# Optimization experiments

Hardware: AMD Instinct MI355X
Metric: run time of the kernel (lower is better)

Reference implementation:

```python
import jax, jax.numpy as jnp
import numpy as np

# ---- static geometry (matches init_kwargs / input_specs) ----
WH, WW = 7, 7            # window_size
H, W = 112, 112          # feature-map size (reshape[1], reshape[2])
NH = 8                   # num_heads
EPS = 1e-5


def _relative_position_index():
    ch, cw = np.arange(WH), np.arange(WW)
    coords = np.stack(np.meshgrid(ch, cw, indexing='ij')).reshape(2, -1)   # (2, S)
    rel = coords[:, :, None] - coords[:, None, :]                          # (2, S, S)
    rel = rel.transpose(1, 2, 0).astype(np.int64)
    rel[..., 0] += WH - 1
    rel[..., 1] += WW - 1
    rel[..., 0] *= 2 * WW - 1
    return rel.sum(-1)                                                     # (S, S)


def _shift_mask():
    h, w = H // WH, W // WW
    s1, s2 = WH - WH // 2, WW - WW // 2
    m = np.zeros((h, w, WH, WW, WH, WW), dtype=bool)
    m[-1, :, :s1, :, s1:, :] = True
    m[-1, :, s1:, :, :s1, :] = True
    m[:, -1, :, :s2, :, s2:] = True
    m[:, -1, :, s2:, :, :s2] = True
    return m.reshape(1, 1, h * w, WH * WW, WH * WW)                        # (1,1,N,S,S)


REL_IDX = jnp.asarray(_relative_position_index())
ATTN_MASK = jnp.asarray(_shift_mask())


def layernorm(x, g, b):
    mu = x.mean(-1, keepdims=True)
    var = jnp.mean(jnp.square(x - mu), -1, keepdims=True)
    return (x - mu) * jax.lax.rsqrt(var + EPS) * g + b


def setup_inputs() -> dict:
    key = jax.random.key(0)
    ks = jax.random.split(key, 8)
    B, N, S, C = 8, 256, 49, 256
    d = {
        'x': jax.random.normal(ks[0], (B, N, S, C), jnp.float32),
        'reshape': jnp.array([B, H, W, C], jnp.int64),
        'norm1_g': jnp.ones((C,), jnp.float32),
        'norm1_b': jnp.zeros((C,), jnp.float32),
        'qkv_w': jax.random.normal(ks[1], (3 * C, C), jnp.float32) * 0.02,
        'qkv_b': jnp.zeros((3 * C,), jnp.float32),
        'proj_w': jax.random.normal(ks[2], (C, C), jnp.float32) * 0.02,
        'proj_b': jnp.zeros((C,), jnp.float32),
        'norm2_g': jnp.ones((C,), jnp.float32),
        'norm2_b': jnp.zeros((C,), jnp.float32),
        'mlp_w1': jax.random.normal(ks[3], (4 * C, C), jnp.float32) * 0.02,
        'mlp_b1': jnp.zeros((4 * C,), jnp.float32),
        'mlp_w2': jax.random.normal(ks[4], (C, 4 * C), jnp.float32) * 0.02,
        'mlp_b2': jnp.zeros((C,), jnp.float32),
        'bias_table': jax.random.normal(ks[5], ((2 * WH - 1) * (2 * WW - 1), NH), jnp.float32) * 0.02,
    }
    return d


def reference(x, reshape, norm1_g, norm1_b, qkv_w, qkv_b, proj_w, proj_b,
              norm2_g, norm2_b, mlp_w1, mlp_b1, mlp_w2, mlp_b2, bias_table):
    B, N, S, C = x.shape
    hd = C // NH
    scale = hd ** -0.5

    shortcut = x
    h = layernorm(x, norm1_g, norm1_b)
    qkv = h @ qkv_w.T + qkv_b                                   # (B,N,S,3C)
    qkv = qkv.reshape(B, N, S, 3, NH, hd).transpose(3, 0, 4, 1, 2, 5)
    q, k, v = qkv[0], qkv[1], qkv[2]                            # (B,NH,N,S,hd)

    attn = jnp.einsum('bhnsd,bhntd->bhnst', q * scale, k)       # (B,NH,N,S,S)
    bias = bias_table[REL_IDX]                                  # (S,S,NH) gather
    attn = attn + bias.transpose(2, 0, 1)[None, :, None]        # +(1,NH,1,S,S)
    attn = jnp.where(ATTN_MASK, -jnp.inf, attn)                 # type=='S' mask
    attn = jax.nn.softmax(attn, axis=-1)

    out = jnp.einsum('bhnst,bhntd->bhnsd', attn, v)             # (B,NH,N,S,hd)
    out = out.transpose(0, 2, 3, 1, 4).reshape(B, N, S, C)
    out = out @ proj_w.T + proj_b

    x = shortcut + out
    h2 = layernorm(x, norm2_g, norm2_b)
    mlp = jax.nn.gelu(h2 @ mlp_w1.T + mlp_b1, approximate=False) @ mlp_w2.T + mlp_b2
    return x + mlp
```

## Files before the change

### kernel.cpp

```cpp
#include <hip/hip_runtime.h>
#include <hip/hip_bf16.h>
#include <math.h>

#define R_TOTAL 100352
#define CDIM    256
#define NWIN    2048
#define NHEAD   8
#define HD      32
#define SW      49

typedef short s8v  __attribute__((ext_vector_type(8)));
typedef float f32x4 __attribute__((ext_vector_type(4)));

__device__ __forceinline__ unsigned short f2bf(float f) {
    __hip_bfloat16 h = __float2bfloat16(f);
    return *reinterpret_cast<unsigned short*>(&h);
}

__device__ __forceinline__ void gload_lds16(const void* g, void* lds) {
    __builtin_amdgcn_global_load_lds(
        (const __attribute__((address_space(1))) void*)g,
        (__attribute__((address_space(3))) void*)lds, 16, 0, 0);
}

__global__ void cvt_f32_bf16(const float* __restrict__ in,
                             unsigned short* __restrict__ out, int n4) {
    int i = blockIdx.x * blockDim.x + threadIdx.x;
    if (i < n4) {
        float4 v = ((const float4*)in)[i];
        unsigned short o[4] = {f2bf(v.x), f2bf(v.y), f2bf(v.z), f2bf(v.w)};
        ((uint2*)out)[i] = *(uint2*)o;
    }
}

__global__ __launch_bounds__(256)
void ln_rows(const float* __restrict__ in, const float* __restrict__ g,
             const float* __restrict__ b, unsigned short* __restrict__ out,
             int rows) {
    int wid = threadIdx.x >> 6, lane = threadIdx.x & 63;
    int row = blockIdx.x * 4 + wid;
    if (row >= rows) return;
    const float4 v = *(const float4*)(in + (size_t)row * CDIM + lane * 4);
    float s = v.x + v.y + v.z + v.w;
#pragma unroll
    for (int t = 1; t < 64; t <<= 1) s += __shfl_xor(s, t);
    float mean = s * (1.0f / 256.0f);
    float dx = v.x - mean, dy = v.y - mean, dz = v.z - mean, dw = v.w - mean;
    float q = dx * dx + dy * dy + dz * dz + dw * dw;
#pragma unroll
    for (int t = 1; t < 64; t <<= 1) q += __shfl_xor(q, t);
    float r = rsqrtf(q * (1.0f / 256.0f) + 1e-5f);
    const float4 gg = *(const float4*)(g + lane * 4);
    const float4 bb = *(const float4*)(b + lane * 4);
    unsigned short o[4] = {f2bf(dx * r * gg.x + bb.x), f2bf(dy * r * gg.y + bb.y),
                           f2bf(dz * r * gg.z + bb.z), f2bf(dw * r * gg.w + bb.w)};
    *(uint2*)(out + (size_t)row * CDIM + lane * 4) = *(uint2*)o;
}

template <int EPI>
__global__ __launch_bounds__(256)
void gemm_nt(const unsigned short* __restrict__ A, const unsigned short* __restrict__ B,
             const float* __restrict__ bias, const float* __restrict__ resid,
             void* __restrict__ outp, int M, int N, int K) {
    constexpr int BM = 128, BN = 128, BK = 32;
    __shared__ unsigned short As[BM][BK];
    __shared__ unsigned short Bs[BN][BK];

    const int tiles_n = N / BN;
    const int bm = blockIdx.x / tiles_n;
    const int bn = blockIdx.x % tiles_n;
    const int tid = threadIdx.x;
    const int wid = tid >> 6;
    const int lane = tid & 63;
    const int wr = wid >> 1, wc = wid & 1;
    const int fr = lane & 15;
    const int kc = lane >> 4;

    f32x4 acc[4][4] = {};

    const int srow = wid * 16 + (lane >> 2);
    const int scol = (lane & 3) * 8;
    const unsigned short* Abase = A + (size_t)(bm * BM) * K + scol;
    const unsigned short* Bbase = B + (size_t)(bn * BN) * K + scol;
    char* AsB = (char*)&As[0][0];
    char* BsB = (char*)&Bs[0][0];
    const int lbase = wid * 1024;

    for (int kt = 0; kt < K; kt += BK) {
        gload_lds16(Abase + (size_t)srow * K + kt,        AsB + lbase);
        gload_lds16(Abase + (size_t)(srow + 64) * K + kt, AsB + 4096 + lbase);
        gload_lds16(Bbase + (size_t)srow * K + kt,        BsB + lbase);
        gload_lds16(Bbase + (size_t)(srow + 64) * K + kt, BsB + 4096 + lbase);
        __syncthreads();
        s8v af[4], bfr[4];
#pragma unroll
        for (int i = 0; i < 4; ++i) af[i]  = *(const s8v*)&As[wr * 64 + i * 16 + fr][kc * 8];
#pragma unroll
        for (int j = 0; j < 4; ++j) bfr[j] = *(const s8v*)&Bs[wc * 64 + j * 16 + fr][kc * 8];
#pragma unroll
        for (int i = 0; i < 4; ++i)
#pragma unroll
            for (int j = 0; j < 4; ++j)
                acc[i][j] = __builtin_amdgcn_mfma_f32_16x16x32_bf16(af[i], bfr[j], acc[i][j], 0, 0, 0);
        __syncthreads();
    }

    const int m0 = bm * BM + wr * 64;
    const int n0 = bn * BN + wc * 64;
#pragma unroll
    for (int i = 0; i < 4; ++i) {
#pragma unroll
        for (int j = 0; j < 4; ++j) {
#pragma unroll
            for (int v = 0; v < 4; ++v) {
                const int m = m0 + i * 16 + kc * 4 + v;
                const int n = n0 + j * 16 + fr;
                float val = acc[i][j][v] + bias[n];
                if constexpr (EPI == 0) {
                    const int part = n >> 8;
                    const int c = n & 255;
                    const int head = c >> 5;
                    const int dd = c & 31;
                    const int win = m / SW;
                    const int s = m - win * SW;
                    ((unsigned short*)outp)[(size_t)part * ((size_t)NWIN * NHEAD * SW * HD)
                        + (((size_t)(win * NHEAD + head) * SW + s) * HD) + dd] = f2bf(val);
                } else if constexpr (EPI == 1) {
                    ((float*)outp)[(size_t)m * CDIM + n] = val + resid[(size_t)m * CDIM + n];
                } else if constexpr (EPI == 2) {
                    float gv = 0.5f * val * (1.0f + erff(val * 0.70710678118654752f));
                    ((unsigned short*)outp)[(size_t)m * 1024 + n] = f2bf(gv);
                } else {
                    ((float*)outp)[(size_t)m * CDIM + n] = val + resid[(size_t)m * CDIM + n];
                }
            }
        }
    }
}

__global__ __launch_bounds__(64)
void attn_win(const unsigned short* __restrict__ qkv,
              const float* __restrict__ btab,
              unsigned short* __restrict__ outp)
{
    __shared__ unsigned short Vt[32][72];
    __shared__ unsigned short Ps[64][72];
    __shared__ float bcol[169];

    const int wh = blockIdx.x;
    const int win = wh >> 3;
    const int head = wh & 7;
    const int lane = threadIdx.x;
    const size_t s3 = (size_t)NWIN * NHEAD * SW * HD;
    const size_t base = (size_t)wh * (SW * HD);

    for (int t = lane; t < 169; t += 64) bcol[t] = btab[t * NHEAD + head];

    {
        const int r = lane;
        if (r < SW) {
            const int4* v4 = (const int4*)(qkv + 2 * s3 + base + (size_t)r * HD);
            int4 vt[4];
#pragma unroll
            for (int c = 0; c < 4; ++c) vt[c] = v4[c];
            const unsigned short* vr = (const unsigned short*)vt;
#pragma unroll
            for (int d = 0; d < 32; ++d) Vt[d][r] = vr[d];
        } else {
#pragma unroll
            for (int d = 0; d < 32; ++d) Vt[d][r] = 0;
        }
    }

    const int fr = lane & 15, kc = lane >> 4;

    s8v qa[4], kb[4];
    {
        const unsigned short* Qg = qkv + base;
        const unsigned short* Kg = qkv + s3 + base;
#pragma unroll
        for (int i = 0; i < 4; ++i)
            qa[i] = *(const s8v*)(Qg + (size_t)(i * 16 + fr) * HD + kc * 8);
#pragma unroll
        for (int j = 0; j < 4; ++j)
            kb[j] = *(const s8v*)(Kg + (size_t)(j * 16 + fr) * HD + kc * 8);
    }

    f32x4 sc[4][4] = {};
#pragma unroll
    for (int i = 0; i < 4; ++i)
#pragma unroll
        for (int j = 0; j < 4; ++j)
            sc[i][j] = __builtin_amdgcn_mfma_f32_16x16x32_bf16(qa[i], kb[j], sc[i][j], 0, 0, 0);

    __syncthreads();

    const float scale = 0.17677669529663687f;
    const int nwin = win & 255;
    const bool lastrow = ((nwin >> 4) == 15);
    const bool lastcol = ((nwin & 15) == 15);

    int cj[4];
    bool jh4[4], jw4[4], jvalid[4];
#pragma unroll
    for (int tj = 0; tj < 4; ++tj) {
        const int j = tj * 16 + fr;
        const int jh = j / 7, jw = j - jh * 7;
        jvalid[tj] = (j < SW);
        cj[tj] = jh * 13 + jw;
        jh4[tj] = (jh < 4);
        jw4[tj] = (jw < 4);
    }

#pragma unroll
    for (int ti = 0; ti < 4; ++ti) {
#pragma unroll
        for (int v = 0; v < 4; ++v) {
            const int i = ti * 16 + kc * 4 + v;
            const int ih = i / 7, iw = i - ih * 7;
            const bool ivalid = (i < SW);
            const int ci = ih * 13 + iw;
            const bool ih4 = (ih < 4), iw4 = (iw < 4);
            float vals[4];
#pragma unroll
            for (int tj = 0; tj < 4; ++tj) {
                const bool ok = ivalid && jvalid[tj];
                const int bidx = ok ? (ci - cj[tj] + 84) : 0;
                const float bv = bcol[bidx];
                const bool msk = (lastrow && (ih4 != jh4[tj])) ||
                                 (lastcol && (iw4 != jw4[tj]));
                const float s = sc[ti][tj][v] * scale + bv;
                vals[tj] = (ok && !msk) ? s : -1e30f;
            }
            float mx = fmaxf(fmaxf(vals[0], vals[1]), fmaxf(vals[2], vals[3]));
#pragma unroll
            for (int t = 1; t < 16; t <<= 1) mx = fmaxf(mx, __shfl_xor(mx, t));
            float e[4], sum = 0.0f;
#pragma unroll
            for (int tj = 0; tj < 4; ++tj) { e[tj] = __expf(vals[tj] - mx); sum += e[tj]; }
#pragma unroll
            for (int t = 1; t < 16; t <<= 1) sum += __shfl_xor(sum, t);
            const float inv = 1.0f / sum;
#pragma unroll
            for (int tj = 0; tj < 4; ++tj)
                Ps[i][tj * 16 + fr] = f2bf(e[tj] * inv);
        }
    }
    __syncthreads();

    f32x4 oa[4][2] = {};
#pragma unroll
    for (int ks = 0; ks < 2; ++ks) {
        s8v pa[4], vb[2];
#pragma unroll
        for (int ti = 0; ti < 4; ++ti) pa[ti] = *(const s8v*)&Ps[ti * 16 + fr][ks * 32 + kc * 8];
#pragma unroll
        for (int tj = 0; tj < 2; ++tj) vb[tj] = *(const s8v*)&Vt[tj * 16 + fr][ks * 32 + kc * 8];
#pragma unroll
        for (int ti = 0; ti < 4; ++ti)
#pragma unroll
            for (int tj = 0; tj < 2; ++tj)
                oa[ti][tj] = __builtin_amdgcn_mfma_f32_16x16x32_bf16(pa[ti], vb[tj], oa[ti][tj], 0, 0, 0);
    }

#pragma unroll
    for (int ti = 0; ti < 4; ++ti)
#pragma unroll
        for (int tj = 0; tj < 2; ++tj)
#pragma unroll
            for (int v = 0; v < 4; ++v) {
                const int i = ti * 16 + kc * 4 + v;
                if (i < SW) {
                    const int d = tj * 16 + fr;
                    outp[((size_t)win * SW + i) * CDIM + head * HD + d] = f2bf(oa[ti][tj][v]);
                }
            }
}

extern "C" void kernel_launch(void* const* d_in, const int* in_sizes, int n_in,
                              void* d_out, int out_size, void* d_ws, size_t ws_size,
                              hipStream_t stream) {
    const float* x       = (const float*)d_in[0];
    const float* n1g     = (const float*)d_in[2];
    const float* n1b     = (const float*)d_in[3];
    const float* qkv_w   = (const float*)d_in[4];
    const float* qkv_b   = (const float*)d_in[5];
    const float* proj_w  = (const float*)d_in[6];
    const float* proj_b  = (const float*)d_in[7];
    const float* n2g     = (const float*)d_in[8];
    const float* n2b     = (const float*)d_in[9];
    const float* mlp_w1  = (const float*)d_in[10];
    const float* mlp_b1  = (const float*)d_in[11];
    const float* mlp_w2  = (const float*)d_in[12];
    const float* mlp_b2  = (const float*)d_in[13];
    const float* btab    = (const float*)d_in[14];

    const int R = R_TOTAL;

    char* w = (char*)d_ws;
    unsigned short* wqkv  = (unsigned short*)w; w += (size_t)768 * 256 * 2;
    unsigned short* wproj = (unsigned short*)w; w += (size_t)256 * 256 * 2;
    unsigned short* wm1   = (unsigned short*)w; w += (size_t)1024 * 256 * 2;
    unsigned short* wm2   = (unsigned short*)w; w += (size_t)256 * 1024 * 2;
    unsigned short* hbuf  = (unsigned short*)w; w += (size_t)R * CDIM * 2;
    unsigned short* qkvb  = (unsigned short*)w;
    unsigned short* hid   = qkvb;               w += (size_t)3 * R * CDIM * 2;
    unsigned short* attno = (unsigned short*)w; w += (size_t)R * CDIM * 2;
    float*          x2    = (float*)w;          w += (size_t)R * CDIM * 4;
    unsigned short* h2    = hbuf;

    cvt_f32_bf16<<<192, 256, 0, stream>>>(qkv_w,  wqkv, 49152);
    cvt_f32_bf16<<<64,  256, 0, stream>>>(proj_w, wproj, 16384);
    cvt_f32_bf16<<<256, 256, 0, stream>>>(mlp_w1, wm1, 65536);
    cvt_f32_bf16<<<256, 256, 0, stream>>>(mlp_w2, wm2, 65536);

    ln_rows<<<R / 4, 256, 0, stream>>>(x, n1g, n1b, hbuf, R);

    gemm_nt<0><<<784 * 6, 256, 0, stream>>>(hbuf, wqkv, qkv_b, nullptr, qkvb, R, 768, 256);

    attn_win<<<NWIN * NHEAD, 64, 0, stream>>>(qkvb, btab, attno);

    gemm_nt<1><<<784 * 2, 256, 0, stream>>>(attno, wproj, proj_b, x, x2, R, 256, 256);

    ln_rows<<<R / 4, 256, 0, stream>>>(x2, n2g, n2b, h2, R);

    gemm_nt<2><<<784 * 8, 256, 0, stream>>>(h2, wm1, mlp_b1, nullptr, hid, R, 1024, 256);

    gemm_nt<3><<<784 * 2, 256, 0, stream>>>(hid, wm2, mlp_b2, x2, (float*)d_out, R, 256, 1024);
}
```

Baseline: 751.5 us.

## Double-buffer GEMM LDS tiles and swizzle block order across XCDs

```diff
diff --git a/kernel.cpp b/kernel.cpp
--- a/kernel.cpp
+++ b/kernel.cpp
@@ -58,17 +58,22 @@
 }
 
 template <int EPI>
-__global__ __launch_bounds__(256)
+__global__ __launch_bounds__(256, 4)
 void gemm_nt(const unsigned short* __restrict__ A, const unsigned short* __restrict__ B,
              const float* __restrict__ bias, const float* __restrict__ resid,
              void* __restrict__ outp, int M, int N, int K) {
     constexpr int BM = 128, BN = 128, BK = 32;
-    __shared__ unsigned short As[BM][BK];
-    __shared__ unsigned short Bs[BN][BK];
+    __shared__ unsigned short As[2][BM][BK];
+    __shared__ unsigned short Bs[2][BN][BK];
+
+    const int nwg = gridDim.x;
+    const int cpx = nwg >> 3;
+    const int bid = blockIdx.x;
+    const int swz = (bid & 7) * cpx + (bid >> 3);
 
     const int tiles_n = N / BN;
-    const int bm = blockIdx.x / tiles_n;
-    const int bn = blockIdx.x % tiles_n;
+    const int bm = swz / tiles_n;
+    const int bn = swz % tiles_n;
     const int tid = threadIdx.x;
     const int wid = tid >> 6;
     const int lane = tid & 63;
@@ -82,28 +87,41 @@
     const int scol = (lane & 3) * 8;
     const unsigned short* Abase = A + (size_t)(bm * BM) * K + scol;
     const unsigned short* Bbase = B + (size_t)(bn * BN) * K + scol;
-    char* AsB = (char*)&As[0][0];
-    char* BsB = (char*)&Bs[0][0];
+    char* AsB = (char*)&As[0][0][0];
+    char* BsB = (char*)&Bs[0][0][0];
     const int lbase = wid * 1024;
 
-    for (int kt = 0; kt < K; kt += BK) {
-        gload_lds16(Abase + (size_t)srow * K + kt,        AsB + lbase);
-        gload_lds16(Abase + (size_t)(srow + 64) * K + kt, AsB + 4096 + lbase);
-        gload_lds16(Bbase + (size_t)srow * K + kt,        BsB + lbase);
-        gload_lds16(Bbase + (size_t)(srow + 64) * K + kt, BsB + 4096 + lbase);
-        __syncthreads();
+    auto stage = [&](int buf, int kt) {
+        char* Ad = AsB + buf * 8192 + lbase;
+        char* Bd = BsB + buf * 8192 + lbase;
+        gload_lds16(Abase + (size_t)srow * K + kt,        Ad);
+        gload_lds16(Abase + (size_t)(srow + 64) * K + kt, Ad + 4096);
+        gload_lds16(Bbase + (size_t)srow * K + kt,        Bd);
+        gload_lds16(Bbase + (size_t)(srow + 64) * K + kt, Bd + 4096);
+    };
+    auto compute = [&](int buf) {
         s8v af[4], bfr[4];
 #pragma unroll
-        for (int i = 0; i < 4; ++i) af[i]  = *(const s8v*)&As[wr * 64 + i * 16 + fr][kc * 8];
-#pragma unroll
-        for (int j = 0; j < 4; ++j) bfr[j] = *(const s8v*)&Bs[wc * 64 + j * 16 + fr][kc * 8];
+        for (int i = 0; i < 4; ++i) af[i]  = *(const s8v*)&As[buf][wr * 64 + i * 16 + fr][kc * 8];
+#pragma unroll
+        for (int j = 0; j < 4; ++j) bfr[j] = *(const s8v*)&Bs[buf][wc * 64 + j * 16 + fr][kc * 8];
 #pragma unroll
         for (int i = 0; i < 4; ++i)
 #pragma unroll
             for (int j = 0; j < 4; ++j)
                 acc[i][j] = __builtin_amdgcn_mfma_f32_16x16x32_bf16(af[i], bfr[j], acc[i][j], 0, 0, 0);
+    };
+
+    stage(0, 0);
+    __syncthreads();
+    int cur = 0;
+    for (int kt = BK; kt < K; kt += BK) {
+        stage(cur ^ 1, kt);
+        compute(cur);
         __syncthreads();
-    }
+        cur ^= 1;
+    }
+    compute(cur);
 
     const int m0 = bm * BM + wr * 64;
     const int n0 = bn * BN + wc * 64;
```

Measured after the change: 663.7 us. 1.13x faster.
